# Performance work log

Hardware: AMD Instinct MI355X
Metric: run time of the kernel (lower is better)

## Reference

```python
import jax, jax.numpy as jnp
import numpy as np
from jax import lax

B_, C_, H_, W_ = 2, 128, 64, 64
N_LAYERS = 2
D_STATE = 16
D_INNER = 2 * C_          # mamba expand=2
D_CONV = 4
DT_RANK = (C_ + 15) // 16  # ceil(d_model/16) = 8


def _layernorm(x, g, b, eps=1e-5):
    m = jnp.mean(x, axis=-1, keepdims=True)
    v = jnp.mean(jnp.square(x - m), axis=-1, keepdims=True)
    return (x - m) * lax.rsqrt(v + eps) * g + b


def _mamba(x, in_w, conv_w, conv_b, xproj_w, dt_w, dt_b, A_log, ssm_D, out_w):
    # x: (B, L, C)
    B, L, C = x.shape
    di, N = A_log.shape
    R = dt_w.shape[1]
    xz = x @ in_w.T                              # (B, L, 2*di)
    u, z = jnp.split(xz, 2, axis=-1)
    # causal depthwise conv1d, kernel d_conv, left-pad d_conv-1
    uc = u.transpose(0, 2, 1)                    # (B, di, L)
    uc = lax.conv_general_dilated(uc, conv_w, (1,), [(D_CONV - 1, 0)],
                                  feature_group_count=di)
    uc = uc + conv_b[None, :, None]
    u = jax.nn.silu(uc.transpose(0, 2, 1))       # (B, L, di)
    dbl = u @ xproj_w.T                          # (B, L, R+2N)
    dt, Bm, Cm = jnp.split(dbl, [R, R + N], axis=-1)
    dt = jax.nn.softplus(dt @ dt_w.T + dt_b)     # (B, L, di)
    A = -jnp.exp(A_log)                          # (di, N)
    dA = jnp.exp(dt[..., None] * A)              # (B, L, di, N)
    dBu = (dt * u)[..., None] * Bm[:, :, None, :]  # (B, L, di, N)

    def step(h, inp):
        dA_t, dBu_t, C_t = inp
        h = dA_t * h + dBu_t                     # (B, di, N)
        y = jnp.einsum('bdn,bn->bd', h, C_t)
        return h, y

    h0 = jnp.zeros((B, di, N), x.dtype)
    _, ys = lax.scan(step, h0, (dA.transpose(1, 0, 2, 3),
                                dBu.transpose(1, 0, 2, 3),
                                Cm.transpose(1, 0, 2)))
    y = ys.transpose(1, 0, 2) + u * ssm_D        # (B, L, di)
    y = y * jax.nn.silu(z)
    return y @ out_w.T                           # (B, L, C)


def setup_inputs() -> dict:
    key = jax.random.key(0)
    ks = jax.random.split(key, 24)
    C, di, N, R, L4 = C_, D_INNER, D_STATE, DT_RANK, 4 * C_
    s = lambda f: 1.0 / np.sqrt(f)
    inp = {
        'x': jax.random.normal(ks[0], (B_, C_, H_, W_), jnp.float32),
        'embed_w': jax.random.normal(ks[1], (C, C), jnp.float32) * s(C),
        'embed_b': jnp.zeros((C,), jnp.float32),
        'outc_w': jax.random.normal(ks[2], (C, C), jnp.float32) * s(C),
        'outc_b': jnp.zeros((C,), jnp.float32),
        'ln_g': jnp.ones((N_LAYERS, C), jnp.float32),
        'ln_b': jnp.zeros((N_LAYERS, C), jnp.float32),
        'in_w': jax.random.normal(ks[3], (N_LAYERS, 2 * di, C), jnp.float32) * s(C),
        'conv_w': jax.random.normal(ks[4], (N_LAYERS, di, 1, D_CONV), jnp.float32) * s(D_CONV),
        'conv_b': jnp.zeros((N_LAYERS, di), jnp.float32),
        'xproj_w': jax.random.normal(ks[5], (N_LAYERS, R + 2 * N, di), jnp.float32) * s(di),
        'dtproj_w': jax.random.normal(ks[6], (N_LAYERS, di, R), jnp.float32) * s(R),
        'dtproj_b': jax.random.uniform(ks[7], (N_LAYERS, di), jnp.float32, -4.0, -2.0),
        'A_log': jnp.tile(jnp.log(jnp.arange(1, N + 1, dtype=jnp.float32))[None, None, :],
                          (N_LAYERS, di, 1)),
        'ssm_D': jnp.ones((N_LAYERS, di), jnp.float32),
        'mout_w': jax.random.normal(ks[8], (N_LAYERS, C, di), jnp.float32) * s(di),
        'ffn_w1': jax.random.normal(ks[9], (N_LAYERS, L4, C), jnp.float32) * s(C),
        'ffn_b1': jnp.zeros((N_LAYERS, L4), jnp.float32),
        'ffn_w2': jax.random.normal(ks[10], (N_LAYERS, C, L4), jnp.float32) * s(L4),
        'ffn_b2': jnp.zeros((N_LAYERS, C), jnp.float32),
    }
    return inp


def reference(x, embed_w, embed_b, outc_w, outc_b, ln_g, ln_b, in_w, conv_w,
              conv_b, xproj_w, dtproj_w, dtproj_b, A_log, ssm_D, mout_w,
              ffn_w1, ffn_b1, ffn_w2, ffn_b2):
    B, C, H, W = x.shape
    residual = x
    h = jnp.einsum('bchw,oc->bohw', x, embed_w) + embed_b[None, :, None, None]
    t = h.reshape(B, C, H * W).transpose(0, 2, 1)   # (B, L, C)
    for i in range(N_LAYERS):
        r = t
        t2 = _layernorm(t, ln_g[i], ln_b[i])
        t2 = _mamba(t2, in_w[i], conv_w[i], conv_b[i], xproj_w[i],
                    dtproj_w[i], dtproj_b[i], A_log[i], ssm_D[i], mout_w[i])
        t = t2 + r
        r = t
        t2 = _layernorm(t, ln_g[i], ln_b[i])  # same LN params reused (as in source)
        t2 = jax.nn.gelu(t2 @ ffn_w1[i].T + ffn_b1[i], approximate=False)
        t2 = t2 @ ffn_w2[i].T + ffn_b2[i]
        t = t2 + r
    y = t.transpose(0, 2, 1).reshape(B, C, H, W)
    y = jnp.einsum('bchw,oc->bohw', y, outc_w) + outc_b[None, :, None, None]
    return residual + y
```

## Files before the change

### kernel.cpp

```cpp
#include <hip/hip_runtime.h>
#include <hip/hip_bf16.h>


#define LSEQ 4096
#define BLC  8192
#define NC   64
#define CHK  64
#define NCH  8192

typedef __attribute__((ext_vector_type(4))) float f32x4;
typedef __attribute__((ext_vector_type(8))) short s16x8;

__device__ __forceinline__ unsigned short f2bu(float f) {
    unsigned u = __float_as_uint(f);
    return (unsigned short)((u + 0x7fffu + ((u >> 16) & 1u)) >> 16);
}
__device__ __forceinline__ float softplus_f(float v) {
    return (v > 0.f) ? v + log1pf(expf(-v)) : log1pf(expf(v));
}

template<bool ADD>
__global__ __launch_bounds__(256) void transpose_kernel(
    const float* __restrict__ in_, float* __restrict__ out_,
    const float* __restrict__ add, int R, int Cc)
{
    __shared__ float tile[32][33];
    size_t boff = (size_t)blockIdx.z * R * Cc;
    int r0 = blockIdx.y * 32, c0 = blockIdx.x * 32;
    int tx = threadIdx.x, ty = threadIdx.y;
#pragma unroll
    for (int j = 0; j < 4; ++j)
        tile[ty + j * 8][tx] = in_[boff + (size_t)(r0 + ty + j * 8) * Cc + (c0 + tx)];
    __syncthreads();
#pragma unroll
    for (int j = 0; j < 4; ++j) {
        size_t idx = boff + (size_t)(c0 + ty + j * 8) * R + (r0 + tx);
        float v = tile[tx][ty + j * 8];
        if (ADD) v += add[idx];
        out_[idx] = v;
    }
}

__global__ __launch_bounds__(256) void build_wcomb(
    const float* __restrict__ xproj_w, const float* __restrict__ dtproj_w,
    float* __restrict__ wc)
{
    int i = blockIdx.x * 256 + threadIdx.x;
    int layer = i / 81920;
    int rem   = i - layer * 81920;
    int row = rem >> 8, col = rem & 255;
    const float* xp = xproj_w + layer * 10240;
    float v = 0.f;
    if (row < 256) {
        const float* dw = dtproj_w + layer * 2048 + row * 8;
#pragma unroll
        for (int r = 0; r < 8; ++r) v = fmaf(dw[r], xp[r * 256 + col], v);
    } else if (row < 288) {
        v = xp[(8 + row - 256) * 256 + col];
    }
    wc[i] = v;
}

template<int BM, int ACT, bool BIAS, bool RES, bool EPI>
__global__ __launch_bounds__(256) void mgemm(
    const float* __restrict__ X, const float* __restrict__ W,
    const float* __restrict__ bias, const float* __restrict__ res,
    const float* __restrict__ pu, const float* __restrict__ pz,
    const float* __restrict__ pD,
    float* __restrict__ Y, int N, int K)
{
    constexpr int MF = BM / 32;
    __shared__ __align__(16) unsigned short Xs[BM * 64];
    __shared__ __align__(16) unsigned short Ws[64 * 64];
    int tid  = threadIdx.x;
    int lane = tid & 63;
    int wave = tid >> 6;
    int wm = wave >> 1, wn = wave & 1;
    int l15 = lane & 15, l4 = lane >> 4;
    int bm = blockIdx.x * BM, bn = blockIdx.y * 64;
    f32x4 acc[MF][2] = {};
    int q  = tid & 15;
    int r0 = tid >> 4;

    for (int k0 = 0; k0 < K; k0 += 64) {
        __syncthreads();
#pragma unroll
        for (int p = 0; p < BM / 16; ++p) {
            int row = r0 + p * 16;
            size_t gi = (size_t)(bm + row) * K + k0 + q * 4;
            float4 v = *(const float4*)&X[gi];
            if (EPI) {
                float4 u4 = *(const float4*)&pu[gi];
                float4 z4 = *(const float4*)&pz[gi];
                float4 D4 = *(const float4*)&pD[k0 + q * 4];
                v.x = fmaf(u4.x, D4.x, v.x) * (z4.x / (1.f + __expf(-z4.x)));
                v.y = fmaf(u4.y, D4.y, v.y) * (z4.y / (1.f + __expf(-z4.y)));
                v.z = fmaf(u4.z, D4.z, v.z) * (z4.z / (1.f + __expf(-z4.z)));
                v.w = fmaf(u4.w, D4.w, v.w) * (z4.w / (1.f + __expf(-z4.w)));
            }
            unsigned lo = f2bu(v.x) | ((unsigned)f2bu(v.y) << 16);
            unsigned hi = f2bu(v.z) | ((unsigned)f2bu(v.w) << 16);
            int off = (row * 128 + q * 8) ^ ((row & 7) << 4);
            *(uint2*)((char*)Xs + off) = make_uint2(lo, hi);
        }
#pragma unroll
        for (int p = 0; p < 4; ++p) {
            int row = r0 + p * 16;
            float4 v = *(const float4*)&W[(size_t)(bn + row) * K + k0 + q * 4];
            unsigned lo = f2bu(v.x) | ((unsigned)f2bu(v.y) << 16);
            unsigned hi = f2bu(v.z) | ((unsigned)f2bu(v.w) << 16);
            int off = (row * 128 + q * 8) ^ ((row & 7) << 4);
            *(uint2*)((char*)Ws + off) = make_uint2(lo, hi);
        }
        __syncthreads();
#pragma unroll
        for (int ks = 0; ks < 2; ++ks) {
            s16x8 a[MF], b[2];
#pragma unroll
            for (int mf = 0; mf < MF; ++mf) {
                int row = wm * (BM / 2) + mf * 16 + l15;
                int off = (row * 128 + (ks * 32 + l4 * 8) * 2) ^ ((row & 7) << 4);
                a[mf] = *(const s16x8*)((const char*)Xs + off);
            }
#pragma unroll
            for (int nf = 0; nf < 2; ++nf) {
                int row = wn * 32 + nf * 16 + l15;
                int off = (row * 128 + (ks * 32 + l4 * 8) * 2) ^ ((row & 7) << 4);
                b[nf] = *(const s16x8*)((const char*)Ws + off);
            }
#pragma unroll
            for (int mf = 0; mf < MF; ++mf)
#pragma unroll
                for (int nf = 0; nf < 2; ++nf)
                    acc[mf][nf] = __builtin_amdgcn_mfma_f32_16x16x32_bf16(
                        a[mf], b[nf], acc[mf][nf], 0, 0, 0);
        }
    }

#pragma unroll
    for (int mf = 0; mf < MF; ++mf) {
#pragma unroll
        for (int nf = 0; nf < 2; ++nf) {
            int col   = bn + wn * 32 + nf * 16 + l15;
            int rbase = bm + wm * (BM / 2) + mf * 16 + l4 * 4;
            float bv = BIAS ? bias[col] : 0.f;
#pragma unroll
            for (int r = 0; r < 4; ++r) {
                float v = acc[mf][nf][r] + bv;
                if (ACT == 2) v = 0.5f * v * (1.f + erff(v * 0.70710678118654752f));
                size_t o = (size_t)(rbase + r) * N + col;
                if (RES) v += res[o];
                Y[o] = v;
            }
        }
    }
}

template<int ACT, bool BIAS, bool SPLIT>
__global__ __launch_bounds__(256) void mgemm_ln(
    const float* __restrict__ X,
    const float* __restrict__ lng, const float* __restrict__ lnb,
    const float* __restrict__ W, const float* __restrict__ bias,
    float* __restrict__ Y, float* __restrict__ Y2, int N)
{
    __shared__ __align__(16) unsigned short Xs[128 * 128];
    __shared__ __align__(16) unsigned short Ws[64 * 64];
    int tid  = threadIdx.x;
    int lane = tid & 63;
    int wave = tid >> 6;
    int wm = wave >> 1, wn = wave & 1;
    int l15 = lane & 15, l4 = lane >> 4;
    int bm = blockIdx.x * 128, bn = blockIdx.y * 64;

    int rsub = lane >> 4;
    int cg   = lane & 15;
    float4 ga = *(const float4*)&lng[cg * 8], gb = *(const float4*)&lng[cg * 8 + 4];
    float4 ba = *(const float4*)&lnb[cg * 8], bb2 = *(const float4*)&lnb[cg * 8 + 4];
#pragma unroll 2
    for (int it = 0; it < 8; ++it) {
        int row = wave * 32 + it * 4 + rsub;
        const float* xr = X + (size_t)(bm + row) * 128 + cg * 8;
        float4 xa = *(const float4*)xr;
        float4 xb = *(const float4*)(xr + 4);
        float s = xa.x + xa.y + xa.z + xa.w + xb.x + xb.y + xb.z + xb.w;
        float q = xa.x*xa.x + xa.y*xa.y + xa.z*xa.z + xa.w*xa.w
                + xb.x*xb.x + xb.y*xb.y + xb.z*xb.z + xb.w*xb.w;
        s += __shfl_xor(s, 1, 16); q += __shfl_xor(q, 1, 16);
        s += __shfl_xor(s, 2, 16); q += __shfl_xor(q, 2, 16);
        s += __shfl_xor(s, 4, 16); q += __shfl_xor(q, 4, 16);
        s += __shfl_xor(s, 8, 16); q += __shfl_xor(q, 8, 16);
        float mean = s * 0.0078125f;
        float var  = fmaf(-mean, mean, q * 0.0078125f);
        float rstd = rsqrtf(var + 1e-5f);
        float o0 = fmaf((xa.x - mean) * rstd, ga.x, ba.x);
        float o1 = fmaf((xa.y - mean) * rstd, ga.y, ba.y);
        float o2 = fmaf((xa.z - mean) * rstd, ga.z, ba.z);
        float o3 = fmaf((xa.w - mean) * rstd, ga.w, ba.w);
        float o4 = fmaf((xb.x - mean) * rstd, gb.x, bb2.x);
        float o5 = fmaf((xb.y - mean) * rstd, gb.y, bb2.y);
        float o6 = fmaf((xb.z - mean) * rstd, gb.z, bb2.z);
        float o7 = fmaf((xb.w - mean) * rstd, gb.w, bb2.w);
        uint4 wv;
        wv.x = f2bu(o0) | ((unsigned)f2bu(o1) << 16);
        wv.y = f2bu(o2) | ((unsigned)f2bu(o3) << 16);
        wv.z = f2bu(o4) | ((unsigned)f2bu(o5) << 16);
        wv.w = f2bu(o6) | ((unsigned)f2bu(o7) << 16);
        int off = (row * 256 + cg * 16) ^ ((row & 7) << 4);
        *(uint4*)((char*)Xs + off) = wv;
    }

    f32x4 acc[4][2] = {};
    int q4 = tid & 15, r0 = tid >> 4;
    for (int k0 = 0; k0 < 128; k0 += 64) {
#pragma unroll
        for (int p = 0; p < 4; ++p) {
            int row = r0 + p * 16;
            float4 v = *(const float4*)&W[(size_t)(bn + row) * 128 + k0 + q4 * 4];
            unsigned lo = f2bu(v.x) | ((unsigned)f2bu(v.y) << 16);
            unsigned hi = f2bu(v.z) | ((unsigned)f2bu(v.w) << 16);
            int off = (row * 128 + q4 * 8) ^ ((row & 7) << 4);
            *(uint2*)((char*)Ws + off) = make_uint2(lo, hi);
        }
        __syncthreads();
#pragma unroll
        for (int ks = 0; ks < 2; ++ks) {
            s16x8 a[4], b[2];
#pragma unroll
            for (int mf = 0; mf < 4; ++mf) {
                int row = wm * 64 + mf * 16 + l15;
                int off = (row * 256 + (k0 + ks * 32 + l4 * 8) * 2) ^ ((row & 7) << 4);
                a[mf] = *(const s16x8*)((const char*)Xs + off);
            }
#pragma unroll
            for (int nf = 0; nf < 2; ++nf) {
                int row = wn * 32 + nf * 16 + l15;
                int off = (row * 128 + (ks * 32 + l4 * 8) * 2) ^ ((row & 7) << 4);
                b[nf] = *(const s16x8*)((const char*)Ws + off);
            }
#pragma unroll
            for (int mf = 0; mf < 4; ++mf)
#pragma unroll
                for (int nf = 0; nf < 2; ++nf)
                    acc[mf][nf] = __builtin_amdgcn_mfma_f32_16x16x32_bf16(
                        a[mf], b[nf], acc[mf][nf], 0, 0, 0);
        }
        __syncthreads();
    }

#pragma unroll
    for (int mf = 0; mf < 4; ++mf) {
#pragma unroll
        for (int nf = 0; nf < 2; ++nf) {
            int col   = bn + wn * 32 + nf * 16 + l15;
            int rbase = bm + wm * 64 + mf * 16 + l4 * 4;
            float bv = BIAS ? bias[col] : 0.f;
#pragma unroll
            for (int r = 0; r < 4; ++r) {
                float v = acc[mf][nf][r] + bv;
                if (ACT == 2) v = 0.5f * v * (1.f + erff(v * 0.70710678118654752f));
                if (SPLIT) {
                    if (col < 256) Y [(size_t)(rbase + r) * 256 + col]       = v;
                    else           Y2[(size_t)(rbase + r) * 256 + col - 256] = v;
                } else {
                    Y[(size_t)(rbase + r) * N + col] = v;
                }
            }
        }
    }
}

__global__ __launch_bounds__(256) void mgemm_dtbc(
    const float* __restrict__ Xu, const float* __restrict__ W,
    const float* __restrict__ bias,
    float* __restrict__ dtT, float* __restrict__ dtuT, float* __restrict__ bct)
{
    __shared__ __align__(16) unsigned short Xs[128 * 64];
    __shared__ __align__(16) unsigned short Ws[64 * 64];
    int tid  = threadIdx.x;
    int lane = tid & 63;
    int wave = tid >> 6;
    int wm = wave >> 1, wn = wave & 1;
    int l15 = lane & 15, l4 = lane >> 4;
    int bm = blockIdx.x * 128, bn = blockIdx.y * 64;
    f32x4 acc[4][2] = {};
    int q  = tid & 15;
    int r0 = tid >> 4;

    for (int k0 = 0; k0 < 256; k0 += 64) {
        __syncthreads();
#pragma unroll
        for (int p = 0; p < 8; ++p) {
            int row = r0 + p * 16;
            float4 v = *(const float4*)&Xu[(size_t)(bm + row) * 256 + k0 + q * 4];
            unsigned lo = f2bu(v.x) | ((unsigned)f2bu(v.y) << 16);
            unsigned hi = f2bu(v.z) | ((unsigned)f2bu(v.w) << 16);
            int off = (row * 128 + q * 8) ^ ((row & 7) << 4);
            *(uint2*)((char*)Xs + off) = make_uint2(lo, hi);
        }
#pragma unroll
        for (int p = 0; p < 4; ++p) {
            int row = r0 + p * 16;
            float4 v = *(const float4*)&W[(size_t)(bn + row) * 256 + k0 + q * 4];
            unsigned lo = f2bu(v.x) | ((unsigned)f2bu(v.y) << 16);
            unsigned hi = f2bu(v.z) | ((unsigned)f2bu(v.w) << 16);
            int off = (row * 128 + q * 8) ^ ((row & 7) << 4);
            *(uint2*)((char*)Ws + off) = make_uint2(lo, hi);
        }
        __syncthreads();
#pragma unroll
        for (int ks = 0; ks < 2; ++ks) {
            s16x8 a[4], b[2];
#pragma unroll
            for (int mf = 0; mf < 4; ++mf) {
                int row = wm * 64 + mf * 16 + l15;
                int off = (row * 128 + (ks * 32 + l4 * 8) * 2) ^ ((row & 7) << 4);
                a[mf] = *(const s16x8*)((const char*)Xs + off);
            }
#pragma unroll
            for (int nf = 0; nf < 2; ++nf) {
                int row = wn * 32 + nf * 16 + l15;
                int off = (row * 128 + (ks * 32 + l4 * 8) * 2) ^ ((row & 7) << 4);
                b[nf] = *(const s16x8*)((const char*)Ws + off);
            }
#pragma unroll
            for (int mf = 0; mf < 4; ++mf)
#pragma unroll
                for (int nf = 0; nf < 2; ++nf)
                    acc[mf][nf] = __builtin_amdgcn_mfma_f32_16x16x32_bf16(
                        a[mf], b[nf], acc[mf][nf], 0, 0, 0);
        }
    }

    if (bn < 256) {
#pragma unroll
        for (int mf = 0; mf < 4; ++mf) {
#pragma unroll
            for (int nf = 0; nf < 2; ++nf) {
                int col   = bn + wn * 32 + nf * 16 + l15;
                int rbase = bm + wm * 64 + mf * 16 + l4 * 4;
                float bv = bias[col];
                float4 uu;
                uu.x = Xu[(size_t)(rbase + 0) * 256 + col];
                uu.y = Xu[(size_t)(rbase + 1) * 256 + col];
                uu.z = Xu[(size_t)(rbase + 2) * 256 + col];
                uu.w = Xu[(size_t)(rbase + 3) * 256 + col];
                float4 dtv, duv;
                float v0 = softplus_f(acc[mf][nf][0] + bv);
                float v1 = softplus_f(acc[mf][nf][1] + bv);
                float v2 = softplus_f(acc[mf][nf][2] + bv);
                float v3 = softplus_f(acc[mf][nf][3] + bv);
                dtv = make_float4(v0, v1, v2, v3);
                duv = make_float4(v0 * uu.x, v1 * uu.y, v2 * uu.z, v3 * uu.w);
                *(float4*)&dtT [(size_t)col * BLC + rbase] = dtv;
                *(float4*)&dtuT[(size_t)col * BLC + rbase] = duv;
            }
        }
    } else {
#pragma unroll
        for (int mf = 0; mf < 4; ++mf) {
#pragma unroll
            for (int nf = 0; nf < 2; ++nf) {
                int col16 = wn * 32 + nf * 16 + l15;
                int rbase = bm + wm * 64 + mf * 16 + l4 * 4;
                if (col16 < 32) {
                    float4 v = make_float4(acc[mf][nf][0], acc[mf][nf][1],
                                           acc[mf][nf][2], acc[mf][nf][3]);
                    *(float4*)&bct[(size_t)col16 * BLC + rbase] = v;
                }
            }
        }
    }
}

__global__ __launch_bounds__(256) void conv_silu_kernel(
    const float* __restrict__ u, const float* __restrict__ cw,
    const float* __restrict__ cb, float* __restrict__ out)
{
    int i   = blockIdx.x * 256 + threadIdx.x;
    int dq  = (i & 63) << 2;
    int row = i >> 6;
    int l   = row & (LSEQ - 1);
    float4 a = *(const float4*)&cb[dq];
    float w[4][4];
#pragma unroll
    for (int e = 0; e < 4; ++e) {
        float4 we = *(const float4*)&cw[(dq + e) * 4];
        w[e][0] = we.x; w[e][1] = we.y; w[e][2] = we.z; w[e][3] = we.w;
    }
#pragma unroll
    for (int j = 0; j < 4; ++j) {
        if (l >= 3 - j) {
            const float4 v = *(const float4*)&u[(size_t)(row - 3 + j) * 256 + dq];
            a.x = fmaf(v.x, w[0][j], a.x);
            a.y = fmaf(v.y, w[1][j], a.y);
            a.z = fmaf(v.z, w[2][j], a.z);
            a.w = fmaf(v.w, w[3][j], a.w);
        }
    }
    float4 o;
    o.x = a.x / (1.f + __expf(-a.x));
    o.y = a.y / (1.f + __expf(-a.y));
    o.z = a.z / (1.f + __expf(-a.z));
    o.w = a.w / (1.f + __expf(-a.w));
    *(float4*)&out[(size_t)row * 256 + dq] = o;
}

__global__ __launch_bounds__(256) void scan_phase1(
    const float* __restrict__ dtT, const float* __restrict__ dtuT,
    const float* __restrict__ bct, const float* __restrict__ A_log,
    float* __restrict__ hend, float* __restrict__ aprod)
{
    int g    = threadIdx.x & 3;
    int dloc = threadIdx.x >> 2;
    int d    = blockIdx.x * 64 + dloc;
    int c    = blockIdx.y;
    int b    = blockIdx.z;
    float4 al = *(const float4*)&A_log[d * 16 + g * 4];
    float A0 = -__expf(al.x), A1 = -__expf(al.y), A2 = -__expf(al.z), A3 = -__expf(al.w);
    int base   = d * BLC + b * LSEQ + c * CHK;
    int btbase = b * LSEQ + c * CHK;
    const float* B0p = bct + (size_t)(g * 4 + 0) * BLC + btbase;
    const float* B1p = B0p + BLC;
    const float* B2p = B1p + BLC;
    const float* B3p = B2p + BLC;
    float h0 = 0.f, h1 = 0.f, h2 = 0.f, h3 = 0.f;
    float p0 = 1.f, p1 = 1.f, p2 = 1.f, p3 = 1.f;
#pragma unroll 2
    for (int t4 = 0; t4 < CHK; t4 += 4) {
        float4 dt4 = *(const float4*)&dtT [base + t4];
        float4 du4 = *(const float4*)&dtuT[base + t4];
        float4 B0 = *(const float4*)(B0p + t4);
        float4 B1 = *(const float4*)(B1p + t4);
        float4 B2 = *(const float4*)(B2p + t4);
        float4 B3 = *(const float4*)(B3p + t4);
        float dts[4] = {dt4.x, dt4.y, dt4.z, dt4.w};
        float dus[4] = {du4.x, du4.y, du4.z, du4.w};
        float b0[4] = {B0.x, B0.y, B0.z, B0.w};
        float b1[4] = {B1.x, B1.y, B1.z, B1.w};
        float b2[4] = {B2.x, B2.y, B2.z, B2.w};
        float b3[4] = {B3.x, B3.y, B3.z, B3.w};
#pragma unroll
        for (int j = 0; j < 4; ++j) {
            float a0 = __expf(dts[j] * A0), a1 = __expf(dts[j] * A1);
            float a2 = __expf(dts[j] * A2), a3 = __expf(dts[j] * A3);
            h0 = fmaf(a0, h0, dus[j] * b0[j]); p0 *= a0;
            h1 = fmaf(a1, h1, dus[j] * b1[j]); p1 *= a1;
            h2 = fmaf(a2, h2, dus[j] * b2[j]); p2 *= a2;
            h3 = fmaf(a3, h3, dus[j] * b3[j]); p3 *= a3;
        }
    }
    int ch = (b * 256 + d) * 16 + g * 4;
    *(float4*)&hend [c * NCH + ch] = make_float4(h0, h1, h2, h3);
    *(float4*)&aprod[c * NCH + ch] = make_float4(p0, p1, p2, p3);
}

__global__ __launch_bounds__(256) void scan_phase2(
    const float* __restrict__ hend, float* __restrict__ apr_h0)
{
    int ch = blockIdx.x * 256 + threadIdx.x;
    float h = 0.f;
#pragma unroll
    for (int c = 0; c < NC; ++c) {
        float ap = apr_h0[c * NCH + ch];
        float he = hend[c * NCH + ch];
        apr_h0[c * NCH + ch] = h;
        h = fmaf(ap, h, he);
    }
}

__global__ __launch_bounds__(256) void scan_phase3(
    const float* __restrict__ dtT, const float* __restrict__ dtuT,
    const float* __restrict__ bct, const float* __restrict__ A_log,
    const float* __restrict__ h0b, float* __restrict__ y)
{
    int g    = threadIdx.x & 3;
    int dloc = threadIdx.x >> 2;
    int d    = blockIdx.x * 64 + dloc;
    int c    = blockIdx.y;
    int b    = blockIdx.z;
    float4 al = *(const float4*)&A_log[d * 16 + g * 4];
    float A0 = -__expf(al.x), A1 = -__expf(al.y), A2 = -__expf(al.z), A3 = -__expf(al.w);
    int base   = d * BLC + b * LSEQ + c * CHK;
    int row0   = b * LSEQ + c * CHK;
    const float* B0p = bct + (size_t)(g * 4 + 0) * BLC + row0;
    const float* B1p = B0p + BLC;
    const float* B2p = B1p + BLC;
    const float* B3p = B2p + BLC;
    const float* C0p = bct + (size_t)(16 + g * 4) * BLC + row0;
    const float* C1p = C0p + BLC;
    const float* C2p = C1p + BLC;
    const float* C3p = C2p + BLC;
    int ch = (b * 256 + d) * 16 + g * 4;
    float4 hv = *(const float4*)&h0b[c * NCH + ch];
    float h0 = hv.x, h1 = hv.y, h2 = hv.z, h3 = hv.w;
#pragma unroll 2
    for (int t4 = 0; t4 < CHK; t4 += 4) {
        float4 dt4 = *(const float4*)&dtT [base + t4];
        float4 du4 = *(const float4*)&dtuT[base + t4];
        float4 B0 = *(const float4*)(B0p + t4);
        float4 B1 = *(const float4*)(B1p + t4);
        float4 B2 = *(const float4*)(B2p + t4);
        float4 B3 = *(const float4*)(B3p + t4);
        float4 C0 = *(const float4*)(C0p + t4);
        float4 C1 = *(const float4*)(C1p + t4);
        float4 C2 = *(const float4*)(C2p + t4);
        float4 C3 = *(const float4*)(C3p + t4);
        float dts[4] = {dt4.x, dt4.y, dt4.z, dt4.w};
        float dus[4] = {du4.x, du4.y, du4.z, du4.w};
        float b0[4] = {B0.x, B0.y, B0.z, B0.w};
        float b1[4] = {B1.x, B1.y, B1.z, B1.w};
        float b2[4] = {B2.x, B2.y, B2.z, B2.w};
        float b3[4] = {B3.x, B3.y, B3.z, B3.w};
        float c0[4] = {C0.x, C0.y, C0.z, C0.w};
        float c1[4] = {C1.x, C1.y, C1.z, C1.w};
        float c2[4] = {C2.x, C2.y, C2.z, C2.w};
        float c3[4] = {C3.x, C3.y, C3.z, C3.w};
#pragma unroll
        for (int j = 0; j < 4; ++j) {
            float a0 = __expf(dts[j] * A0), a1 = __expf(dts[j] * A1);
            float a2 = __expf(dts[j] * A2), a3 = __expf(dts[j] * A3);
            h0 = fmaf(a0, h0, dus[j] * b0[j]);
            h1 = fmaf(a1, h1, dus[j] * b1[j]);
            h2 = fmaf(a2, h2, dus[j] * b2[j]);
            h3 = fmaf(a3, h3, dus[j] * b3[j]);
            float p = h0 * c0[j];
            p = fmaf(h1, c1[j], p);
            p = fmaf(h2, c2[j], p);
            p = fmaf(h3, c3[j], p);
            p += __shfl_xor(p, 1);
            p += __shfl_xor(p, 2);
            if (g == 0) y[(size_t)(row0 + t4 + j) * 256 + d] = p;
        }
    }
}

extern "C" void kernel_launch(void* const* d_in, const int* in_sizes, int n_in,
                              void* d_out, int out_size, void* d_ws, size_t ws_size,
                              hipStream_t stream)
{
    const float* x        = (const float*)d_in[0];
    const float* embed_w  = (const float*)d_in[1];
    const float* embed_b  = (const float*)d_in[2];
    const float* outc_w   = (const float*)d_in[3];
    const float* outc_b   = (const float*)d_in[4];
    const float* ln_g     = (const float*)d_in[5];
    const float* ln_b     = (const float*)d_in[6];
    const float* in_w     = (const float*)d_in[7];
    const float* conv_w   = (const float*)d_in[8];
    const float* conv_b   = (const float*)d_in[9];
    const float* xproj_w  = (const float*)d_in[10];
    const float* dtproj_w = (const float*)d_in[11];
    const float* dtproj_b = (const float*)d_in[12];
    const float* A_log    = (const float*)d_in[13];
    const float* ssm_D    = (const float*)d_in[14];
    const float* mout_w   = (const float*)d_in[15];
    const float* ffn_w1   = (const float*)d_in[16];
    const float* ffn_b1   = (const float*)d_in[17];
    const float* ffn_w2   = (const float*)d_in[18];
    const float* ffn_b2   = (const float*)d_in[19];

    float* ws    = (float*)d_ws;
    float* t     = ws;
    float* tmp2  = ws + 1048576;
    float* ub    = ws + 3145728;
    float* zb    = ws + 5242880;
    float* ucv   = ws + 7340032;
    float* dtb   = ws + 9437184;
    float* bct   = ws + 11534336;
    float* hend  = ws + 11796480;
    float* apr   = ws + 12320768;
    float* wcomb = ws + 12845056;
    float* out   = (float*)d_out;

    float* dtT    = ub;
    float* dtuT   = tmp2;
    float* ffnmid = ub;

    dim3 tb(32, 8);
    build_wcomb<<<640, 256, 0, stream>>>(xproj_w, dtproj_w, wcomb);
    transpose_kernel<false><<<dim3(128, 4, 2), tb, 0, stream>>>(x, tmp2, nullptr, 128, 4096);
    mgemm<64, 0, true, false, false><<<dim3(128, 2), 256, 0, stream>>>(
        tmp2, embed_w, embed_b, nullptr, nullptr, nullptr, nullptr, t, 128, 128);

    for (int i = 0; i < 2; ++i) {
        mgemm_ln<0, false, true><<<dim3(64, 8), 256, 0, stream>>>(
            t, ln_g + i * 128, ln_b + i * 128, in_w + i * 65536, nullptr, ub, zb, 512);
        conv_silu_kernel<<<2048, 256, 0, stream>>>(ub, conv_w + i * 1024, conv_b + i * 256, ucv);
        mgemm_dtbc<<<dim3(64, 5), 256, 0, stream>>>(
            ucv, wcomb + i * 81920, dtproj_b + i * 256, dtT, dtuT, bct);
        scan_phase1<<<dim3(4, NC, 2), 256, 0, stream>>>(dtT, dtuT, bct, A_log + i * 4096, hend, apr);
        scan_phase2<<<32, 256, 0, stream>>>(hend, apr);
        scan_phase3<<<dim3(4, NC, 2), 256, 0, stream>>>(dtT, dtuT, bct, A_log + i * 4096, apr, dtb);
        mgemm<64, 0, false, true, true><<<dim3(128, 2), 256, 0, stream>>>(
            dtb, mout_w + i * 32768, nullptr, t, ucv, zb, ssm_D + i * 256, t, 128, 256);
        mgemm_ln<2, true, false><<<dim3(64, 8), 256, 0, stream>>>(
            t, ln_g + i * 128, ln_b + i * 128, ffn_w1 + i * 65536, ffn_b1 + i * 512, ffnmid, nullptr, 512);
        mgemm<64, 0, true, true, false><<<dim3(128, 2), 256, 0, stream>>>(
            ffnmid, ffn_w2 + i * 65536, ffn_b2 + i * 128, t, nullptr, nullptr, nullptr, t, 128, 512);
    }

    mgemm<64, 0, true, false, false><<<dim3(128, 2), 256, 0, stream>>>(
        t, outc_w, outc_b, nullptr, nullptr, nullptr, nullptr, tmp2, 128, 128);
    transpose_kernel<true><<<dim3(4, 128, 2), tb, 0, stream>>>(tmp2, out, x, 4096, 128);
}
```

Before: 427.4 us.

## Widen GEMM N-tiles, shrink scan chunks, fold phase2 and output transpose

```diff
diff --git a/kernel.cpp b/kernel.cpp
--- a/kernel.cpp
+++ b/kernel.cpp
@@ -4,8 +4,8 @@
 
 #define LSEQ 4096
 #define BLC  8192
-#define NC   64
-#define CHK  64
+#define NC   128
+#define CHK  32
 #define NCH  8192
 
 typedef __attribute__((ext_vector_type(4))) float f32x4;
@@ -19,10 +19,8 @@
     return (v > 0.f) ? v + log1pf(expf(-v)) : log1pf(expf(v));
 }
 
-template<bool ADD>
 __global__ __launch_bounds__(256) void transpose_kernel(
-    const float* __restrict__ in_, float* __restrict__ out_,
-    const float* __restrict__ add, int R, int Cc)
+    const float* __restrict__ in_, float* __restrict__ out_, int R, int Cc)
 {
     __shared__ float tile[32][33];
     size_t boff = (size_t)blockIdx.z * R * Cc;
@@ -33,12 +31,8 @@
         tile[ty + j * 8][tx] = in_[boff + (size_t)(r0 + ty + j * 8) * Cc + (c0 + tx)];
     __syncthreads();
 #pragma unroll
-    for (int j = 0; j < 4; ++j) {
-        size_t idx = boff + (size_t)(c0 + ty + j * 8) * R + (r0 + tx);
-        float v = tile[tx][ty + j * 8];
-        if (ADD) v += add[idx];
-        out_[idx] = v;
-    }
+    for (int j = 0; j < 4; ++j)
+        out_[boff + (size_t)(c0 + ty + j * 8) * R + (r0 + tx)] = tile[tx][ty + j * 8];
 }
 
 __global__ __launch_bounds__(256) void build_wcomb(
@@ -46,8 +40,8 @@
     float* __restrict__ wc)
 {
     int i = blockIdx.x * 256 + threadIdx.x;
-    int layer = i / 81920;
-    int rem   = i - layer * 81920;
+    int layer = i / 98304;
+    int rem   = i - layer * 98304;
     int row = rem >> 8, col = rem & 255;
     const float* xp = xproj_w + layer * 10240;
     float v = 0.f;
@@ -61,7 +55,7 @@
     wc[i] = v;
 }
 
-template<int BM, int ACT, bool BIAS, bool RES, bool EPI>
+template<int BM, int BN, int ACT, bool BIAS, bool RES, bool EPI, bool OUTT>
 __global__ __launch_bounds__(256) void mgemm(
     const float* __restrict__ X, const float* __restrict__ W,
     const float* __restrict__ bias, const float* __restrict__ res,
@@ -69,16 +63,16 @@
     const float* __restrict__ pD,
     float* __restrict__ Y, int N, int K)
 {
-    constexpr int MF = BM / 32;
+    constexpr int MF = BM / 32, NF = BN / 32;
     __shared__ __align__(16) unsigned short Xs[BM * 64];
-    __shared__ __align__(16) unsigned short Ws[64 * 64];
+    __shared__ __align__(16) unsigned short Ws[BN * 64];
     int tid  = threadIdx.x;
     int lane = tid & 63;
     int wave = tid >> 6;
     int wm = wave >> 1, wn = wave & 1;
     int l15 = lane & 15, l4 = lane >> 4;
-    int bm = blockIdx.x * BM, bn = blockIdx.y * 64;
-    f32x4 acc[MF][2] = {};
+    int bm = blockIdx.x * BM, bn = blockIdx.y * BN;
+    f32x4 acc[MF][NF] = {};
     int q  = tid & 15;
     int r0 = tid >> 4;
 
@@ -104,7 +98,7 @@
             *(uint2*)((char*)Xs + off) = make_uint2(lo, hi);
         }
 #pragma unroll
-        for (int p = 0; p < 4; ++p) {
+        for (int p = 0; p < BN / 16; ++p) {
             int row = r0 + p * 16;
             float4 v = *(const float4*)&W[(size_t)(bn + row) * K + k0 + q * 4];
             unsigned lo = f2bu(v.x) | ((unsigned)f2bu(v.y) << 16);
@@ -115,7 +109,7 @@
         __syncthreads();
 #pragma unroll
         for (int ks = 0; ks < 2; ++ks) {
-            s16x8 a[MF], b[2];
+            s16x8 a[MF], b[NF];
 #pragma unroll
             for (int mf = 0; mf < MF; ++mf) {
                 int row = wm * (BM / 2) + mf * 16 + l15;
@@ -123,15 +117,15 @@
                 a[mf] = *(const s16x8*)((const char*)Xs + off);
             }
 #pragma unroll
-            for (int nf = 0; nf < 2; ++nf) {
-                int row = wn * 32 + nf * 16 + l15;
+            for (int nf = 0; nf < NF; ++nf) {
+                int row = wn * (BN / 2) + nf * 16 + l15;
                 int off = (row * 128 + (ks * 32 + l4 * 8) * 2) ^ ((row & 7) << 4);
                 b[nf] = *(const s16x8*)((const char*)Ws + off);
             }
 #pragma unroll
             for (int mf = 0; mf < MF; ++mf)
 #pragma unroll
-                for (int nf = 0; nf < 2; ++nf)
+                for (int nf = 0; nf < NF; ++nf)
                     acc[mf][nf] = __builtin_amdgcn_mfma_f32_16x16x32_bf16(
                         a[mf], b[nf], acc[mf][nf], 0, 0, 0);
         }
@@ -140,17 +134,26 @@
 #pragma unroll
     for (int mf = 0; mf < MF; ++mf) {
 #pragma unroll
-        for (int nf = 0; nf < 2; ++nf) {
-            int col   = bn + wn * 32 + nf * 16 + l15;
+        for (int nf = 0; nf < NF; ++nf) {
+            int col   = bn + wn * (BN / 2) + nf * 16 + l15;
             int rbase = bm + wm * (BM / 2) + mf * 16 + l4 * 4;
             float bv = BIAS ? bias[col] : 0.f;
-#pragma unroll
-            for (int r = 0; r < 4; ++r) {
-                float v = acc[mf][nf][r] + bv;
-                if (ACT == 2) v = 0.5f * v * (1.f + erff(v * 0.70710678118654752f));
-                size_t o = (size_t)(rbase + r) * N + col;
-                if (RES) v += res[o];
-                Y[o] = v;
+            if (OUTT) {
+                int bi = rbase >> 12;
+                int l  = rbase & 4095;
+                size_t ob = (size_t)bi * 524288 + (size_t)col * 4096 + l;
+#pragma unroll
+                for (int r = 0; r < 4; ++r)
+                    Y[ob + r] = acc[mf][nf][r] + bv + res[ob + r];
+            } else {
+#pragma unroll
+                for (int r = 0; r < 4; ++r) {
+                    float v = acc[mf][nf][r] + bv;
+                    if (ACT == 2) v = 0.5f * v * (1.f + erff(v * 0.70710678118654752f));
+                    size_t o = (size_t)(rbase + r) * N + col;
+                    if (RES) v += res[o];
+                    Y[o] = v;
+                }
             }
         }
     }
@@ -164,13 +167,13 @@
     float* __restrict__ Y, float* __restrict__ Y2, int N)
 {
     __shared__ __align__(16) unsigned short Xs[128 * 128];
-    __shared__ __align__(16) unsigned short Ws[64 * 64];
+    __shared__ __align__(16) unsigned short Ws[128 * 64];
     int tid  = threadIdx.x;
     int lane = tid & 63;
     int wave = tid >> 6;
     int wm = wave >> 1, wn = wave & 1;
     int l15 = lane & 15, l4 = lane >> 4;
-    int bm = blockIdx.x * 128, bn = blockIdx.y * 64;
+    int bm = blockIdx.x * 128, bn = blockIdx.y * 128;
 
     int rsub = lane >> 4;
     int cg   = lane & 15;
@@ -209,11 +212,11 @@
         *(uint4*)((char*)Xs + off) = wv;
     }
 
-    f32x4 acc[4][2] = {};
+    f32x4 acc[4][4] = {};
     int q4 = tid & 15, r0 = tid >> 4;
     for (int k0 = 0; k0 < 128; k0 += 64) {
 #pragma unroll
-        for (int p = 0; p < 4; ++p) {
+        for (int p = 0; p < 8; ++p) {
             int row = r0 + p * 16;
             float4 v = *(const float4*)&W[(size_t)(bn + row) * 128 + k0 + q4 * 4];
             unsigned lo = f2bu(v.x) | ((unsigned)f2bu(v.y) << 16);
@@ -224,7 +227,7 @@
         __syncthreads();
 #pragma unroll
         for (int ks = 0; ks < 2; ++ks) {
-            s16x8 a[4], b[2];
+            s16x8 a[4], b[4];
 #pragma unroll
             for (int mf = 0; mf < 4; ++mf) {
                 int row = wm * 64 + mf * 16 + l15;
@@ -232,15 +235,15 @@
                 a[mf] = *(const s16x8*)((const char*)Xs + off);
             }
 #pragma unroll
-            for (int nf = 0; nf < 2; ++nf) {
-                int row = wn * 32 + nf * 16 + l15;
+            for (int nf = 0; nf < 4; ++nf) {
+                int row = wn * 64 + nf * 16 + l15;
                 int off = (row * 128 + (ks * 32 + l4 * 8) * 2) ^ ((row & 7) << 4);
                 b[nf] = *(const s16x8*)((const char*)Ws + off);
             }
 #pragma unroll
             for (int mf = 0; mf < 4; ++mf)
 #pragma unroll
-                for (int nf = 0; nf < 2; ++nf)
+                for (int nf = 0; nf < 4; ++nf)
                     acc[mf][nf] = __builtin_amdgcn_mfma_f32_16x16x32_bf16(
                         a[mf], b[nf], acc[mf][nf], 0, 0, 0);
         }
@@ -250,8 +253,8 @@
 #pragma unroll
     for (int mf = 0; mf < 4; ++mf) {
 #pragma unroll
-        for (int nf = 0; nf < 2; ++nf) {
-            int col   = bn + wn * 32 + nf * 16 + l15;
+        for (int nf = 0; nf < 4; ++nf) {
+            int col   = bn + wn * 64 + nf * 16 + l15;
             int rbase = bm + wm * 64 + mf * 16 + l4 * 4;
             float bv = BIAS ? bias[col] : 0.f;
 #pragma unroll
@@ -275,14 +278,14 @@
     float* __restrict__ dtT, float* __restrict__ dtuT, float* __restrict__ bct)
 {
     __shared__ __align__(16) unsigned short Xs[128 * 64];
-    __shared__ __align__(16) unsigned short Ws[64 * 64];
+    __shared__ __align__(16) unsigned short Ws[128 * 64];
     int tid  = threadIdx.x;
     int lane = tid & 63;
     int wave = tid >> 6;
     int wm = wave >> 1, wn = wave & 1;
     int l15 = lane & 15, l4 = lane >> 4;
-    int bm = blockIdx.x * 128, bn = blockIdx.y * 64;
-    f32x4 acc[4][2] = {};
+    int bm = blockIdx.x * 128, bn = blockIdx.y * 128;
+    f32x4 acc[4][4] = {};
     int q  = tid & 15;
     int r0 = tid >> 4;
 
@@ -298,7 +301,7 @@
             *(uint2*)((char*)Xs + off) = make_uint2(lo, hi);
         }
 #pragma unroll
-        for (int p = 0; p < 4; ++p) {
+        for (int p = 0; p < 8; ++p) {
             int row = r0 + p * 16;
             float4 v = *(const float4*)&W[(size_t)(bn + row) * 256 + k0 + q * 4];
             unsigned lo = f2bu(v.x) | ((unsigned)f2bu(v.y) << 16);
@@ -309,7 +312,7 @@
         __syncthreads();
 #pragma unroll
         for (int ks = 0; ks < 2; ++ks) {
-            s16x8 a[4], b[2];
+            s16x8 a[4], b[4];
 #pragma unroll
             for (int mf = 0; mf < 4; ++mf) {
                 int row = wm * 64 + mf * 16 + l15;
@@ -317,26 +320,26 @@
                 a[mf] = *(const s16x8*)((const char*)Xs + off);
             }
 #pragma unroll
-            for (int nf = 0; nf < 2; ++nf) {
-                int row = wn * 32 + nf * 16 + l15;
+            for (int nf = 0; nf < 4; ++nf) {
+                int row = wn * 64 + nf * 16 + l15;
                 int off = (row * 128 + (ks * 32 + l4 * 8) * 2) ^ ((row & 7) << 4);
                 b[nf] = *(const s16x8*)((const char*)Ws + off);
             }
 #pragma unroll
             for (int mf = 0; mf < 4; ++mf)
 #pragma unroll
-                for (int nf = 0; nf < 2; ++nf)
+                for (int nf = 0; nf < 4; ++nf)
                     acc[mf][nf] = __builtin_amdgcn_mfma_f32_16x16x32_bf16(
                         a[mf], b[nf], acc[mf][nf], 0, 0, 0);
         }
     }
 
-    if (bn < 256) {
+    if (blockIdx.y < 2) {
 #pragma unroll
         for (int mf = 0; mf < 4; ++mf) {
 #pragma unroll
-            for (int nf = 0; nf < 2; ++nf) {
-                int col   = bn + wn * 32 + nf * 16 + l15;
+            for (int nf = 0; nf < 4; ++nf) {
+                int col   = bn + wn * 64 + nf * 16 + l15;
                 int rbase = bm + wm * 64 + mf * 16 + l4 * 4;
                 float bv = bias[col];
                 float4 uu;
@@ -344,28 +347,26 @@
                 uu.y = Xu[(size_t)(rbase + 1) * 256 + col];
                 uu.z = Xu[(size_t)(rbase + 2) * 256 + col];
                 uu.w = Xu[(size_t)(rbase + 3) * 256 + col];
-                float4 dtv, duv;
                 float v0 = softplus_f(acc[mf][nf][0] + bv);
                 float v1 = softplus_f(acc[mf][nf][1] + bv);
                 float v2 = softplus_f(acc[mf][nf][2] + bv);
                 float v3 = softplus_f(acc[mf][nf][3] + bv);
-                dtv = make_float4(v0, v1, v2, v3);
-                duv = make_float4(v0 * uu.x, v1 * uu.y, v2 * uu.z, v3 * uu.w);
-                *(float4*)&dtT [(size_t)col * BLC + rbase] = dtv;
-                *(float4*)&dtuT[(size_t)col * BLC + rbase] = duv;
+                *(float4*)&dtT [(size_t)col * BLC + rbase] = make_float4(v0, v1, v2, v3);
+                *(float4*)&dtuT[(size_t)col * BLC + rbase] =
+                    make_float4(v0 * uu.x, v1 * uu.y, v2 * uu.z, v3 * uu.w);
             }
         }
     } else {
 #pragma unroll
         for (int mf = 0; mf < 4; ++mf) {
 #pragma unroll
-            for (int nf = 0; nf < 2; ++nf) {
-                int col16 = wn * 32 + nf * 16 + l15;
+            for (int nf = 0; nf < 4; ++nf) {
+                int col16 = wn * 64 + nf * 16 + l15;
                 int rbase = bm + wm * 64 + mf * 16 + l4 * 4;
                 if (col16 < 32) {
-                    float4 v = make_float4(acc[mf][nf][0], acc[mf][nf][1],
-                                           acc[mf][nf][2], acc[mf][nf][3]);
-                    *(float4*)&bct[(size_t)col16 * BLC + rbase] = v;
+                    *(float4*)&bct[(size_t)col16 * BLC + rbase] =
+                        make_float4(acc[mf][nf][0], acc[mf][nf][1],
+                                    acc[mf][nf][2], acc[mf][nf][3]);
                 }
             }
         }
@@ -454,24 +455,11 @@
     *(float4*)&aprod[c * NCH + ch] = make_float4(p0, p1, p2, p3);
 }
 
-__global__ __launch_bounds__(256) void scan_phase2(
-    const float* __restrict__ hend, float* __restrict__ apr_h0)
-{
-    int ch = blockIdx.x * 256 + threadIdx.x;
-    float h = 0.f;
-#pragma unroll
-    for (int c = 0; c < NC; ++c) {
-        float ap = apr_h0[c * NCH + ch];
-        float he = hend[c * NCH + ch];
-        apr_h0[c * NCH + ch] = h;
-        h = fmaf(ap, h, he);
-    }
-}
-
 __global__ __launch_bounds__(256) void scan_phase3(
     const float* __restrict__ dtT, const float* __restrict__ dtuT,
     const float* __restrict__ bct, const float* __restrict__ A_log,
-    const float* __restrict__ h0b, float* __restrict__ y)
+    const float* __restrict__ hend, const float* __restrict__ aprod,
+    float* __restrict__ y)
 {
     int g    = threadIdx.x & 3;
     int dloc = threadIdx.x >> 2;
@@ -480,8 +468,18 @@
     int b    = blockIdx.z;
     float4 al = *(const float4*)&A_log[d * 16 + g * 4];
     float A0 = -__expf(al.x), A1 = -__expf(al.y), A2 = -__expf(al.z), A3 = -__expf(al.w);
-    int base   = d * BLC + b * LSEQ + c * CHK;
-    int row0   = b * LSEQ + c * CHK;
+    int ch = (b * 256 + d) * 16 + g * 4;
+    float h0 = 0.f, h1 = 0.f, h2 = 0.f, h3 = 0.f;
+    for (int cc = 0; cc < c; ++cc) {
+        float4 ap = *(const float4*)&aprod[cc * NCH + ch];
+        float4 he = *(const float4*)&hend [cc * NCH + ch];
+        h0 = fmaf(ap.x, h0, he.x);
+        h1 = fmaf(ap.y, h1, he.y);
+        h2 = fmaf(ap.z, h2, he.z);
+        h3 = fmaf(ap.w, h3, he.w);
+    }
+    int base = d * BLC + b * LSEQ + c * CHK;
+    int row0 = b * LSEQ + c * CHK;
     const float* B0p = bct + (size_t)(g * 4 + 0) * BLC + row0;
     const float* B1p = B0p + BLC;
     const float* B2p = B1p + BLC;
@@ -490,9 +488,6 @@
     const float* C1p = C0p + BLC;
     const float* C2p = C1p + BLC;
     const float* C3p = C2p + BLC;
-    int ch = (b * 256 + d) * 16 + g * 4;
-    float4 hv = *(const float4*)&h0b[c * NCH + ch];
-    float h0 = hv.x, h1 = hv.y, h2 = hv.z, h3 = hv.w;
 #pragma unroll 2
     for (int t4 = 0; t4 < CHK; t4 += 4) {
         float4 dt4 = *(const float4*)&dtT [base + t4];
@@ -568,8 +563,8 @@
     float* dtb   = ws + 9437184;
     float* bct   = ws + 11534336;
     float* hend  = ws + 11796480;
-    float* apr   = ws + 12320768;
-    float* wcomb = ws + 12845056;
+    float* apr   = ws + 12845056;
+    float* wcomb = ws + 13893632;
     float* out   = (float*)d_out;
 
     float* dtT    = ub;
@@ -577,29 +572,27 @@
     float* ffnmid = ub;
 
     dim3 tb(32, 8);
-    build_wcomb<<<640, 256, 0, stream>>>(xproj_w, dtproj_w, wcomb);
-    transpose_kernel<false><<<dim3(128, 4, 2), tb, 0, stream>>>(x, tmp2, nullptr, 128, 4096);
-    mgemm<64, 0, true, false, false><<<dim3(128, 2), 256, 0, stream>>>(
+    build_wcomb<<<768, 256, 0, stream>>>(xproj_w, dtproj_w, wcomb);
+    transpose_kernel<<<dim3(128, 4, 2), tb, 0, stream>>>(x, tmp2, 128, 4096);
+    mgemm<64, 64, 0, true, false, false, false><<<dim3(128, 2), 256, 0, stream>>>(
         tmp2, embed_w, embed_b, nullptr, nullptr, nullptr, nullptr, t, 128, 128);
 
     for (int i = 0; i < 2; ++i) {
-        mgemm_ln<0, false, true><<<dim3(64, 8), 256, 0, stream>>>(
+        mgemm_ln<0, false, true><<<dim3(64, 4), 256, 0, stream>>>(
             t, ln_g + i * 128, ln_b + i * 128, in_w + i * 65536, nullptr, ub, zb, 512);
         conv_silu_kernel<<<2048, 256, 0, stream>>>(ub, conv_w + i * 1024, conv_b + i * 256, ucv);
-        mgemm_dtbc<<<dim3(64, 5), 256, 0, stream>>>(
-            ucv, wcomb + i * 81920, dtproj_b + i * 256, dtT, dtuT, bct);
+        mgemm_dtbc<<<dim3(64, 3), 256, 0, stream>>>(
+            ucv, wcomb + i * 98304, dtproj_b + i * 256, dtT, dtuT, bct);
         scan_phase1<<<dim3(4, NC, 2), 256, 0, stream>>>(dtT, dtuT, bct, A_log + i * 4096, hend, apr);
-        scan_phase2<<<32, 256, 0, stream>>>(hend, apr);
-        scan_phase3<<<dim3(4, NC, 2), 256, 0, stream>>>(dtT, dtuT, bct, A_log + i * 4096, apr, dtb);
-        mgemm<64, 0, false, true, true><<<dim3(128, 2), 256, 0, stream>>>(
+        scan_phase3<<<dim3(4, NC, 2), 256, 0, stream>>>(dtT, dtuT, bct, A_log + i * 4096, hend, apr, dtb);
+        mgemm<64, 64, 0, false, true, true, false><<<dim3(128, 2), 256, 0, stream>>>(
             dtb, mout_w + i * 32768, nullptr, t, ucv, zb, ssm_D + i * 256, t, 128, 256);
-        mgemm_ln<2, true, false><<<dim3(64, 8), 256, 0, stream>>>(
+        mgemm_ln<2, true, false><<<dim3(64, 4), 256, 0, stream>>>(
             t, ln_g + i * 128, ln_b + i * 128, ffn_w1 + i * 65536, ffn_b1 + i * 512, ffnmid, nullptr, 512);
-        mgemm<64, 0, true, true, false><<<dim3(128, 2), 256, 0, stream>>>(
+        mgemm<64, 64, 0, true, true, false, false><<<dim3(128, 2), 256, 0, stream>>>(
             ffnmid, ffn_w2 + i * 65536, ffn_b2 + i * 128, t, nullptr, nullptr, nullptr, t, 128, 512);
     }
 
-    mgemm<64, 0, true, false, false><<<dim3(128, 2), 256, 0, stream>>>(
-        t, outc_w, outc_b, nullptr, nullptr, nullptr, nullptr, tmp2, 128, 128);
-    transpose_kernel<true><<<dim3(4, 128, 2), tb, 0, stream>>>(tmp2, out, x, 4096, 128);
-}
+    mgemm<64, 64, 0, true, false, false, true><<<dim3(128, 2), 256, 0, stream>>>(
+        t, outc_w, outc_b, x, nullptr, nullptr, nullptr, out, 128, 128);
+}
```

After: 508.1 us. 1.19x slower.
